# Performance work log

Measured on AMD Instinct MI355X. Metric: run time of the kernel, lower is better.

Reference implementation:

```python
import jax, jax.numpy as jnp
import numpy as np

# SMPL-style 22-joint kinematic tree; parents[i] < i for i >= 2 as the module's loop requires.
PARENTS = np.array([-1, 0, 0, 0, 1, 2, 3, 4, 5, 6, 7, 8, 9, 9, 9, 12, 13, 14, 16, 17, 18, 19])
L, J, D6 = 65536, 22, 6


def cont6d_to_mat(d6):
    """6D continuous rotation -> 3x3 rotation matrix (Gram-Schmidt). Columns are b1,b2,b3."""
    a1, a2 = d6[..., :3], d6[..., 3:]
    b1 = a1 / jnp.maximum(jnp.linalg.norm(a1, axis=-1, keepdims=True), 1e-12)
    b2 = a2 - b1 * jnp.sum(b1 * a2, axis=-1, keepdims=True)
    b2 = b2 / jnp.maximum(jnp.linalg.norm(b2, axis=-1, keepdims=True), 1e-12)
    b3 = jnp.cross(b1, b2)
    return jnp.stack((b1, b2, b3), axis=-1)  # (..., 3, 3)


def setup_inputs() -> dict:
    key = jax.random.key(0)
    k1, k2 = jax.random.split(key)
    pred_series = jax.random.normal(k1, (L, J, D6), dtype=jnp.float32)
    offsets = 0.1 * jax.random.normal(k2, (J, 3), dtype=jnp.float32)  # bone offsets (buffer)
    return {"pred_series": pred_series, "offsets": offsets}


def reference(pred_series, offsets):
    # pred_series: (L, 22, 6) -> global positions (L, 22, 3)
    rot_mats = cont6d_to_mat(pred_series)          # (L, 22, 3, 3)

    # Cumulative root rotation: R_t = R_{t-1} @ delta_t, R_{-1} = I  (sequential scan over time)
    deltas = rot_mats[:, 1]                        # (L, 3, 3)
    def step(R, d):
        Rn = R @ d
        return Rn, Rn
    _, R = jax.lax.scan(step, jnp.eye(3, dtype=pred_series.dtype), deltas)  # (L, 3, 3)

    # Root translation: integrate rotated local velocities
    vel_local = pred_series[:, 0, :3]              # (L, 3)
    global_vel = jnp.einsum('tij,tj->ti', R, vel_local)
    root_pos = jnp.cumsum(global_vel, axis=0)      # (L, 3)

    # FK down the static tree, vectorized over time; unrolled over 22 joints (static).
    rots = [None] * J
    pos = [None] * J
    rots[0], pos[0] = R, root_pos
    rots[1] = R
    pos[1] = pos[0] + jnp.einsum('tij,j->ti', R, offsets[1])
    for i in range(2, J):
        p = int(PARENTS[i])
        rots[i] = jnp.einsum('tij,tjk->tik', rots[p], rot_mats[:, i])
        pos[i] = pos[p] + jnp.einsum('tij,j->ti', rots[p], offsets[i])
    return jnp.stack(pos, axis=1)                  # (L, 22, 3)
```

## Files before the change

kernel.cpp:

```cpp
#include <hip/hip_runtime.h>
#include <hip/hip_bf16.h>
#include <stdint.h>


#define LTOT 65536
#define ROW 132
#define P1B 256
#define NBLK (LTOT / P1B)

struct Aff { float A[9]; float b[3]; };

__device__ __forceinline__ void d6_to_mat(float a0, float a1, float a2,
                                          float a3, float a4, float a5,
                                          float R[9]) {
  float n1 = sqrtf(a0 * a0 + a1 * a1 + a2 * a2);
  float i1 = 1.0f / fmaxf(n1, 1e-12f);
  float b10 = a0 * i1, b11 = a1 * i1, b12 = a2 * i1;
  float d = b10 * a3 + b11 * a4 + b12 * a5;
  float c0 = a3 - d * b10, c1 = a4 - d * b11, c2 = a5 - d * b12;
  float n2 = sqrtf(c0 * c0 + c1 * c1 + c2 * c2);
  float i2 = 1.0f / fmaxf(n2, 1e-12f);
  float b20 = c0 * i2, b21 = c1 * i2, b22 = c2 * i2;
  float b30 = b11 * b22 - b12 * b21;
  float b31 = b12 * b20 - b10 * b22;
  float b32 = b10 * b21 - b11 * b20;
  R[0] = b10; R[1] = b20; R[2] = b30;
  R[3] = b11; R[4] = b21; R[5] = b31;
  R[6] = b12; R[7] = b22; R[8] = b32;
}

__device__ __forceinline__ void mat_mul(const float A[9], const float B[9], float C[9]) {
#pragma unroll
  for (int i = 0; i < 3; ++i)
#pragma unroll
    for (int j = 0; j < 3; ++j)
      C[i * 3 + j] = A[i * 3 + 0] * B[0 + j] + A[i * 3 + 1] * B[3 + j] + A[i * 3 + 2] * B[6 + j];
}

__device__ __forceinline__ void mat_vec(const float A[9], float x, float y, float z,
                                        float& ox, float& oy, float& oz) {
  ox = A[0] * x + A[1] * y + A[2] * z;
  oy = A[3] * x + A[4] * y + A[5] * z;
  oz = A[6] * x + A[7] * y + A[8] * z;
}

__device__ __forceinline__ void compose(const Aff& P, const Aff& T, Aff& O) {
  mat_mul(P.A, T.A, O.A);
  float bx, by, bz;
  mat_vec(P.A, T.b[0], T.b[1], T.b[2], bx, by, bz);
  O.b[0] = P.b[0] + bx; O.b[1] = P.b[1] + by; O.b[2] = P.b[2] + bz;
}

__device__ __forceinline__ void aff_identity(Aff& v) {
  v.A[0] = 1.f; v.A[1] = 0.f; v.A[2] = 0.f;
  v.A[3] = 0.f; v.A[4] = 1.f; v.A[5] = 0.f;
  v.A[6] = 0.f; v.A[7] = 0.f; v.A[8] = 1.f;
  v.b[0] = 0.f; v.b[1] = 0.f; v.b[2] = 0.f;
}

__device__ __forceinline__ void wave_scan(Aff& v, int lane) {
#pragma unroll
  for (int s = 1; s < 64; s <<= 1) {
    Aff u;
#pragma unroll
    for (int k = 0; k < 9; ++k) u.A[k] = __shfl_up(v.A[k], s, 64);
#pragma unroll
    for (int k = 0; k < 3; ++k) u.b[k] = __shfl_up(v.b[k], s, 64);
    if (lane >= s) { Aff t; compose(u, v, t); v = t; }
  }
}

__global__ __launch_bounds__(P1B) void fk_phase1(const float* __restrict__ pred,
                                                 float* __restrict__ loc,
                                                 float* __restrict__ agg) {
  int t = blockIdx.x * P1B + threadIdx.x;
  int lane = threadIdx.x & 63, wid = threadIdx.x >> 6;

  const float4* q4 = (const float4*)(pred + (size_t)t * ROW);
  float4 qa = q4[0];
  float4 qb = q4[1];
  float4 qc = q4[2];
  Aff v;
  d6_to_mat(qb.z, qb.w, qc.x, qc.y, qc.z, qc.w, v.A);
  mat_vec(v.A, qa.x, qa.y, qa.z, v.b[0], v.b[1], v.b[2]);

  wave_scan(v, lane);

  __shared__ float sagg[P1B / 64][12];
  if (lane == 63) {
#pragma unroll
    for (int k = 0; k < 9; ++k) sagg[wid][k] = v.A[k];
#pragma unroll
    for (int k = 0; k < 3; ++k) sagg[wid][9 + k] = v.b[k];
  }
  __syncthreads();

  Aff pre; aff_identity(pre);
  for (int w = 0; w < wid; ++w) {
    Aff g, t2;
#pragma unroll
    for (int k = 0; k < 9; ++k) g.A[k] = sagg[w][k];
#pragma unroll
    for (int k = 0; k < 3; ++k) g.b[k] = sagg[w][9 + k];
    compose(pre, g, t2); pre = t2;
  }
  Aff f; compose(pre, v, f);

  float4* o = (float4*)(loc + (size_t)t * 12);
  o[0] = make_float4(f.A[0], f.A[1], f.A[2], f.A[3]);
  o[1] = make_float4(f.A[4], f.A[5], f.A[6], f.A[7]);
  o[2] = make_float4(f.A[8], f.b[0], f.b[1], f.b[2]);
  if (threadIdx.x == P1B - 1) {
    float4* a = (float4*)(agg + (size_t)blockIdx.x * 12);
    a[0] = make_float4(f.A[0], f.A[1], f.A[2], f.A[3]);
    a[1] = make_float4(f.A[4], f.A[5], f.A[6], f.A[7]);
    a[2] = make_float4(f.A[8], f.b[0], f.b[1], f.b[2]);
  }
}

__global__ __launch_bounds__(NBLK) void fk_phase2(const float* __restrict__ agg,
                                                  float* __restrict__ excl) {
  int i = threadIdx.x, lane = i & 63, wid = i >> 6;
  Aff v;
  {
    const float4* a = (const float4*)(agg + (size_t)i * 12);
    float4 a0 = a[0], a1 = a[1], a2 = a[2];
    v.A[0] = a0.x; v.A[1] = a0.y; v.A[2] = a0.z; v.A[3] = a0.w;
    v.A[4] = a1.x; v.A[5] = a1.y; v.A[6] = a1.z; v.A[7] = a1.w;
    v.A[8] = a2.x; v.b[0] = a2.y; v.b[1] = a2.z; v.b[2] = a2.w;
  }
  wave_scan(v, lane);

  __shared__ float sagg[NBLK / 64][12];
  if (lane == 63) {
#pragma unroll
    for (int k = 0; k < 9; ++k) sagg[wid][k] = v.A[k];
#pragma unroll
    for (int k = 0; k < 3; ++k) sagg[wid][9 + k] = v.b[k];
  }
  __syncthreads();

  Aff pre; aff_identity(pre);
  for (int w = 0; w < wid; ++w) {
    Aff g, t2;
#pragma unroll
    for (int k = 0; k < 9; ++k) g.A[k] = sagg[w][k];
#pragma unroll
    for (int k = 0; k < 3; ++k) g.b[k] = sagg[w][9 + k];
    compose(pre, g, t2); pre = t2;
  }
  Aff f; compose(pre, v, f);

  Aff e;
#pragma unroll
  for (int k = 0; k < 9; ++k) e.A[k] = __shfl_up(f.A[k], 1, 64);
#pragma unroll
  for (int k = 0; k < 3; ++k) e.b[k] = __shfl_up(f.b[k], 1, 64);
  if (lane == 0) e = pre;

  float4* o = (float4*)(excl + (size_t)i * 12);
  o[0] = make_float4(e.A[0], e.A[1], e.A[2], e.A[3]);
  o[1] = make_float4(e.A[4], e.A[5], e.A[6], e.A[7]);
  o[2] = make_float4(e.A[8], e.b[0], e.b[1], e.b[2]);
}

__global__ __launch_bounds__(256) void fk_phase3(const float* __restrict__ pred,
                                                 const float* __restrict__ offs,
                                                 const float* __restrict__ loc,
                                                 const float* __restrict__ excl,
                                                 float* __restrict__ out) {
  int t = blockIdx.x * blockDim.x + threadIdx.x;
  const float* lp = loc + (size_t)t * 12;
  const float* ep = excl + (size_t)(t / P1B) * 12;
  float Rl[9], Re[9];
#pragma unroll
  for (int k = 0; k < 9; ++k) { Rl[k] = lp[k]; Re[k] = ep[k]; }
  float R[9];
  mat_mul(Re, Rl, R);
  float rx, ry, rz;
  mat_vec(Re, lp[9], lp[10], lp[11], rx, ry, rz);
  float ov[66];
  ov[0] = ep[9] + rx; ov[1] = ep[10] + ry; ov[2] = ep[11] + rz;

  const float* q = pred + (size_t)t * ROW;

#define CHILD(j, p, Rp)                                                        \
  {                                                                            \
    float ox, oy, oz;                                                          \
    mat_vec(Rp, offs[(j)*3 + 0], offs[(j)*3 + 1], offs[(j)*3 + 2], ox, oy, oz);\
    ov[(j)*3 + 0] = ov[(p)*3 + 0] + ox;                                        \
    ov[(j)*3 + 1] = ov[(p)*3 + 1] + oy;                                        \
    ov[(j)*3 + 2] = ov[(p)*3 + 2] + oz;                                        \
  }
#define ROTJ(j, Rp, Rj)                                                        \
  {                                                                            \
    float Mx[9];                                                               \
    d6_to_mat(q[(j)*6 + 0], q[(j)*6 + 1], q[(j)*6 + 2], q[(j)*6 + 3],          \
              q[(j)*6 + 4], q[(j)*6 + 5], Mx);                                 \
    mat_mul(Rp, Mx, Rj);                                                       \
  }

  CHILD(1, 0, R);
  float r2[9], r3[9], r4[9];
  CHILD(2, 0, R); ROTJ(2, R, r2);
  CHILD(3, 0, R); ROTJ(3, R, r3);
  CHILD(4, 1, R); ROTJ(4, R, r4);
  float r5[9], r6[9], r7[9];
  CHILD(5, 2, r2); ROTJ(5, r2, r5);
  CHILD(6, 3, r3); ROTJ(6, r3, r6);
  CHILD(7, 4, r4); ROTJ(7, r4, r7);
  float r8[9], r9[9];
  CHILD(8, 5, r5); ROTJ(8, r5, r8);
  CHILD(9, 6, r6); ROTJ(9, r6, r9);
  CHILD(10, 7, r7);
  CHILD(11, 8, r8);
  float r12[9], r13[9], r14[9];
  CHILD(12, 9, r9); ROTJ(12, r9, r12);
  CHILD(13, 9, r9); ROTJ(13, r9, r13);
  CHILD(14, 9, r9); ROTJ(14, r9, r14);
  CHILD(15, 12, r12);
  float r16[9], r17[9];
  CHILD(16, 13, r13); ROTJ(16, r13, r16);
  CHILD(17, 14, r14); ROTJ(17, r14, r17);
  float r18[9], r19[9];
  CHILD(18, 16, r16); ROTJ(18, r16, r18);
  CHILD(19, 17, r17); ROTJ(19, r17, r19);
  CHILD(20, 18, r18);
  CHILD(21, 19, r19);

  float2* ob = (float2*)(out + (size_t)t * 66);
#pragma unroll
  for (int k = 0; k < 33; ++k) ob[k] = make_float2(ov[2 * k], ov[2 * k + 1]);
#undef CHILD
#undef ROTJ
}

extern "C" void kernel_launch(void* const* d_in, const int* in_sizes, int n_in,
                              void* d_out, int out_size, void* d_ws, size_t ws_size,
                              hipStream_t stream) {
  const float* pred = (const float*)d_in[0];
  const float* offs = (const float*)d_in[1];
  float* out = (float*)d_out;

  float* ws = (float*)d_ws;
  float* loc  = ws;
  float* agg  = ws + (size_t)12 * LTOT;
  float* excl = ws + (size_t)12 * LTOT + 12 * NBLK;

  fk_phase1<<<NBLK, P1B, 0, stream>>>(pred, loc, agg);
  fk_phase2<<<1, NBLK, 0, stream>>>(agg, excl);
  fk_phase3<<<LTOT / 256, 256, 0, stream>>>(pred, offs, loc, excl, out);
}
```

Measured before the change: 98.90 us.

## Fuse three scan/FK kernels into one cooperative kernel with grid sync

Replaces the three-launch scan pipeline with a single cooperative kernel. Each block computes its local scan, publishes its aggregate, waits at a grid-wide sync, and then redundantly scans all 256 block aggregates in shared memory to get its own prefix before running FK. This drops the per-thread loc buffer round trip and two kernel launches, and it loads the joint 6D values as float2. In exchange every block repeats the aggregate scan, the grid sync must be honoured, and the launch is restricted to one block per CU.

```diff
diff --git a/kernel.cpp b/kernel.cpp
--- a/kernel.cpp
+++ b/kernel.cpp
@@ -1,6 +1,8 @@
 #include <hip/hip_runtime.h>
-#include <hip/hip_bf16.h>
+#include <hip/hip_cooperative_groups.h>
 #include <stdint.h>
+
+namespace cg = cooperative_groups;
 
 
 #define LTOT 65536
@@ -70,11 +72,40 @@
   }
 }
 
-__global__ __launch_bounds__(P1B) void fk_phase1(const float* __restrict__ pred,
-                                                 float* __restrict__ loc,
-                                                 float* __restrict__ agg) {
-  int t = blockIdx.x * P1B + threadIdx.x;
-  int lane = threadIdx.x & 63, wid = threadIdx.x >> 6;
+__device__ __forceinline__ void block_scan(Aff& v, int lane, int wid,
+                                           float (*sagg)[12], Aff& f) {
+  wave_scan(v, lane);
+  if (lane == 63) {
+#pragma unroll
+    for (int k = 0; k < 9; ++k) sagg[wid][k] = v.A[k];
+#pragma unroll
+    for (int k = 0; k < 3; ++k) sagg[wid][9 + k] = v.b[k];
+  }
+  __syncthreads();
+  Aff pre; aff_identity(pre);
+  for (int w = 0; w < wid; ++w) {
+    Aff g, t2;
+#pragma unroll
+    for (int k = 0; k < 9; ++k) g.A[k] = sagg[w][k];
+#pragma unroll
+    for (int k = 0; k < 3; ++k) g.b[k] = sagg[w][9 + k];
+    compose(pre, g, t2); pre = t2;
+  }
+  compose(pre, v, f);
+}
+
+__global__ __launch_bounds__(P1B, 1) void fk_fused(const float* __restrict__ pred,
+                                                   const float* __restrict__ offs,
+                                                   float* __restrict__ agg,
+                                                   float* __restrict__ out) {
+  cg::grid_group grid = cg::this_grid();
+  int tid = threadIdx.x;
+  int t = blockIdx.x * P1B + tid;
+  int lane = tid & 63, wid = tid >> 6;
+
+  __shared__ float sagg1[P1B / 64][12];
+  __shared__ float sagg2[P1B / 64][12];
+  __shared__ float sincl[NBLK][13];
 
   const float4* q4 = (const float4*)(pred + (size_t)t * ROW);
   float4 qa = q4[0];
@@ -84,103 +115,50 @@
   d6_to_mat(qb.z, qb.w, qc.x, qc.y, qc.z, qc.w, v.A);
   mat_vec(v.A, qa.x, qa.y, qa.z, v.b[0], v.b[1], v.b[2]);
 
-  wave_scan(v, lane);
-
-  __shared__ float sagg[P1B / 64][12];
-  if (lane == 63) {
-#pragma unroll
-    for (int k = 0; k < 9; ++k) sagg[wid][k] = v.A[k];
-#pragma unroll
-    for (int k = 0; k < 3; ++k) sagg[wid][9 + k] = v.b[k];
-  }
-  __syncthreads();
-
-  Aff pre; aff_identity(pre);
-  for (int w = 0; w < wid; ++w) {
-    Aff g, t2;
-#pragma unroll
-    for (int k = 0; k < 9; ++k) g.A[k] = sagg[w][k];
-#pragma unroll
-    for (int k = 0; k < 3; ++k) g.b[k] = sagg[w][9 + k];
-    compose(pre, g, t2); pre = t2;
-  }
-  Aff f; compose(pre, v, f);
-
-  float4* o = (float4*)(loc + (size_t)t * 12);
-  o[0] = make_float4(f.A[0], f.A[1], f.A[2], f.A[3]);
-  o[1] = make_float4(f.A[4], f.A[5], f.A[6], f.A[7]);
-  o[2] = make_float4(f.A[8], f.b[0], f.b[1], f.b[2]);
-  if (threadIdx.x == P1B - 1) {
+  Aff f;
+  block_scan(v, lane, wid, sagg1, f);
+
+  if (tid == P1B - 1) {
     float4* a = (float4*)(agg + (size_t)blockIdx.x * 12);
     a[0] = make_float4(f.A[0], f.A[1], f.A[2], f.A[3]);
     a[1] = make_float4(f.A[4], f.A[5], f.A[6], f.A[7]);
     a[2] = make_float4(f.A[8], f.b[0], f.b[1], f.b[2]);
   }
-}
-
-__global__ __launch_bounds__(NBLK) void fk_phase2(const float* __restrict__ agg,
-                                                  float* __restrict__ excl) {
-  int i = threadIdx.x, lane = i & 63, wid = i >> 6;
-  Aff v;
+  __threadfence();
+  grid.sync();
+
+  Aff v2;
   {
-    const float4* a = (const float4*)(agg + (size_t)i * 12);
+    const float4* a = (const float4*)(agg + (size_t)tid * 12);
     float4 a0 = a[0], a1 = a[1], a2 = a[2];
-    v.A[0] = a0.x; v.A[1] = a0.y; v.A[2] = a0.z; v.A[3] = a0.w;
-    v.A[4] = a1.x; v.A[5] = a1.y; v.A[6] = a1.z; v.A[7] = a1.w;
-    v.A[8] = a2.x; v.b[0] = a2.y; v.b[1] = a2.z; v.b[2] = a2.w;
-  }
-  wave_scan(v, lane);
-
-  __shared__ float sagg[NBLK / 64][12];
-  if (lane == 63) {
-#pragma unroll
-    for (int k = 0; k < 9; ++k) sagg[wid][k] = v.A[k];
-#pragma unroll
-    for (int k = 0; k < 3; ++k) sagg[wid][9 + k] = v.b[k];
-  }
+    v2.A[0] = a0.x; v2.A[1] = a0.y; v2.A[2] = a0.z; v2.A[3] = a0.w;
+    v2.A[4] = a1.x; v2.A[5] = a1.y; v2.A[6] = a1.z; v2.A[7] = a1.w;
+    v2.A[8] = a2.x; v2.b[0] = a2.y; v2.b[1] = a2.z; v2.b[2] = a2.w;
+  }
+  Aff incl;
+  block_scan(v2, lane, wid, sagg2, incl);
+#pragma unroll
+  for (int k = 0; k < 9; ++k) sincl[tid][k] = incl.A[k];
+#pragma unroll
+  for (int k = 0; k < 3; ++k) sincl[tid][9 + k] = incl.b[k];
   __syncthreads();
 
-  Aff pre; aff_identity(pre);
-  for (int w = 0; w < wid; ++w) {
-    Aff g, t2;
-#pragma unroll
-    for (int k = 0; k < 9; ++k) g.A[k] = sagg[w][k];
-#pragma unroll
-    for (int k = 0; k < 3; ++k) g.b[k] = sagg[w][9 + k];
-    compose(pre, g, t2); pre = t2;
-  }
-  Aff f; compose(pre, v, f);
-
-  Aff e;
-#pragma unroll
-  for (int k = 0; k < 9; ++k) e.A[k] = __shfl_up(f.A[k], 1, 64);
-#pragma unroll
-  for (int k = 0; k < 3; ++k) e.b[k] = __shfl_up(f.b[k], 1, 64);
-  if (lane == 0) e = pre;
-
-  float4* o = (float4*)(excl + (size_t)i * 12);
-  o[0] = make_float4(e.A[0], e.A[1], e.A[2], e.A[3]);
-  o[1] = make_float4(e.A[4], e.A[5], e.A[6], e.A[7]);
-  o[2] = make_float4(e.A[8], e.b[0], e.b[1], e.b[2]);
-}
-
-__global__ __launch_bounds__(256) void fk_phase3(const float* __restrict__ pred,
-                                                 const float* __restrict__ offs,
-                                                 const float* __restrict__ loc,
-                                                 const float* __restrict__ excl,
-                                                 float* __restrict__ out) {
-  int t = blockIdx.x * blockDim.x + threadIdx.x;
-  const float* lp = loc + (size_t)t * 12;
-  const float* ep = excl + (size_t)(t / P1B) * 12;
-  float Rl[9], Re[9];
-#pragma unroll
-  for (int k = 0; k < 9; ++k) { Rl[k] = lp[k]; Re[k] = ep[k]; }
-  float R[9];
-  mat_mul(Re, Rl, R);
-  float rx, ry, rz;
-  mat_vec(Re, lp[9], lp[10], lp[11], rx, ry, rz);
+  Aff eb;
+  if (blockIdx.x == 0) {
+    aff_identity(eb);
+  } else {
+    const float* sp = sincl[blockIdx.x - 1];
+#pragma unroll
+    for (int k = 0; k < 9; ++k) eb.A[k] = sp[k];
+#pragma unroll
+    for (int k = 0; k < 3; ++k) eb.b[k] = sp[9 + k];
+  }
+
+  Aff g;
+  compose(eb, f, g);
+  const float* R = g.A;
   float ov[66];
-  ov[0] = ep[9] + rx; ov[1] = ep[10] + ry; ov[2] = ep[11] + rz;
+  ov[0] = g.b[0]; ov[1] = g.b[1]; ov[2] = g.b[2];
 
   const float* q = pred + (size_t)t * ROW;
 
@@ -194,9 +172,10 @@
   }
 #define ROTJ(j, Rp, Rj)                                                        \
   {                                                                            \
+    const float2* qq = (const float2*)(q + (j)*6);             \
+    float2 w0 = qq[0], w1 = qq[1], w2 = qq[2];                                 \
     float Mx[9];                                                               \
-    d6_to_mat(q[(j)*6 + 0], q[(j)*6 + 1], q[(j)*6 + 2], q[(j)*6 + 3],          \
-              q[(j)*6 + 4], q[(j)*6 + 5], Mx);                                 \
+    d6_to_mat(w0.x, w0.y, w1.x, w1.y, w2.x, w2.y, Mx);                         \
     mat_mul(Rp, Mx, Rj);                                                       \
   }
 
@@ -241,13 +220,9 @@
   const float* pred = (const float*)d_in[0];
   const float* offs = (const float*)d_in[1];
   float* out = (float*)d_out;
-
-  float* ws = (float*)d_ws;
-  float* loc  = ws;
-  float* agg  = ws + (size_t)12 * LTOT;
-  float* excl = ws + (size_t)12 * LTOT + 12 * NBLK;
-
-  fk_phase1<<<NBLK, P1B, 0, stream>>>(pred, loc, agg);
-  fk_phase2<<<1, NBLK, 0, stream>>>(agg, excl);
-  fk_phase3<<<LTOT / 256, 256, 0, stream>>>(pred, offs, loc, excl, out);
-}
+  float* agg = (float*)d_ws;
+
+  void* args[] = { (void*)&pred, (void*)&offs, (void*)&agg, (void*)&out };
+  hipLaunchCooperativeKernel((void*)fk_fused, dim3(NBLK), dim3(P1B),
+                             args, 0, stream);
+}
```

Measured after the change: 139.5 us. +41.1%, slower.

## Split tree FK pass into five per-chain waves per time step

Applied to the files above, without the earlier changes.

The final forward-kinematics kernel now launches 64x5 thread blocks. Each threadIdx.y row walks one kinematic chain of the skeleton for 64 time steps, instead of one thread evaluating all 22 joints serially. This targets the long dependent chain and high register pressure of the single-thread tree walk, giving more threads and more latency hiding. The cost is redundant work: every chain recomputes the root composition, and two chains recompute the spine joints 3, 6 and 9. Output stores are now scattered scalar writes. The scan kernels are refactored into a shared block_scan helper, and the second-level scan redundantly recomputes the prefix loop.

```diff
diff --git a/kernel.cpp b/kernel.cpp
--- a/kernel.cpp
+++ b/kernel.cpp
@@ -1,12 +1,11 @@
 #include <hip/hip_runtime.h>
-#include <hip/hip_bf16.h>
 #include <stdint.h>
 
 
 #define LTOT 65536
 #define ROW 132
 #define P1B 256
-#define NBLK (LTOT / P1B)
+#define NSCB (LTOT / P1B)
 
 struct Aff { float A[9]; float b[3]; };
 
@@ -70,11 +69,35 @@
   }
 }
 
-__global__ __launch_bounds__(P1B) void fk_phase1(const float* __restrict__ pred,
-                                                 float* __restrict__ loc,
-                                                 float* __restrict__ agg) {
-  int t = blockIdx.x * P1B + threadIdx.x;
-  int lane = threadIdx.x & 63, wid = threadIdx.x >> 6;
+__device__ __forceinline__ void block_scan(Aff& v, int lane, int wid,
+                                           float (*sagg)[12], Aff& f) {
+  wave_scan(v, lane);
+  if (lane == 63) {
+#pragma unroll
+    for (int k = 0; k < 9; ++k) sagg[wid][k] = v.A[k];
+#pragma unroll
+    for (int k = 0; k < 3; ++k) sagg[wid][9 + k] = v.b[k];
+  }
+  __syncthreads();
+  Aff pre; aff_identity(pre);
+  for (int w = 0; w < wid; ++w) {
+    Aff g, t2;
+#pragma unroll
+    for (int k = 0; k < 9; ++k) g.A[k] = sagg[w][k];
+#pragma unroll
+    for (int k = 0; k < 3; ++k) g.b[k] = sagg[w][9 + k];
+    compose(pre, g, t2); pre = t2;
+  }
+  compose(pre, v, f);
+}
+
+__global__ __launch_bounds__(P1B) void fk_scan(const float* __restrict__ pred,
+                                               float* __restrict__ loc,
+                                               float* __restrict__ agg) {
+  int tid = threadIdx.x;
+  int t = blockIdx.x * P1B + tid;
+  int lane = tid & 63, wid = tid >> 6;
+  __shared__ float sagg[P1B / 64][12];
 
   const float4* q4 = (const float4*)(pred + (size_t)t * ROW);
   float4 qa = q4[0];
@@ -83,34 +106,14 @@
   Aff v;
   d6_to_mat(qb.z, qb.w, qc.x, qc.y, qc.z, qc.w, v.A);
   mat_vec(v.A, qa.x, qa.y, qa.z, v.b[0], v.b[1], v.b[2]);
-
-  wave_scan(v, lane);
-
-  __shared__ float sagg[P1B / 64][12];
-  if (lane == 63) {
-#pragma unroll
-    for (int k = 0; k < 9; ++k) sagg[wid][k] = v.A[k];
-#pragma unroll
-    for (int k = 0; k < 3; ++k) sagg[wid][9 + k] = v.b[k];
-  }
-  __syncthreads();
-
-  Aff pre; aff_identity(pre);
-  for (int w = 0; w < wid; ++w) {
-    Aff g, t2;
-#pragma unroll
-    for (int k = 0; k < 9; ++k) g.A[k] = sagg[w][k];
-#pragma unroll
-    for (int k = 0; k < 3; ++k) g.b[k] = sagg[w][9 + k];
-    compose(pre, g, t2); pre = t2;
-  }
-  Aff f; compose(pre, v, f);
+  Aff f;
+  block_scan(v, lane, wid, sagg, f);
 
   float4* o = (float4*)(loc + (size_t)t * 12);
   o[0] = make_float4(f.A[0], f.A[1], f.A[2], f.A[3]);
   o[1] = make_float4(f.A[4], f.A[5], f.A[6], f.A[7]);
   o[2] = make_float4(f.A[8], f.b[0], f.b[1], f.b[2]);
-  if (threadIdx.x == P1B - 1) {
+  if (tid == P1B - 1) {
     float4* a = (float4*)(agg + (size_t)blockIdx.x * 12);
     a[0] = make_float4(f.A[0], f.A[1], f.A[2], f.A[3]);
     a[1] = make_float4(f.A[4], f.A[5], f.A[6], f.A[7]);
@@ -118,8 +121,8 @@
   }
 }
 
-__global__ __launch_bounds__(NBLK) void fk_phase2(const float* __restrict__ agg,
-                                                  float* __restrict__ excl) {
+__global__ __launch_bounds__(NSCB) void fk_scan2(const float* __restrict__ agg,
+                                                 float* __restrict__ excl) {
   int i = threadIdx.x, lane = i & 63, wid = i >> 6;
   Aff v;
   {
@@ -129,17 +132,9 @@
     v.A[4] = a1.x; v.A[5] = a1.y; v.A[6] = a1.z; v.A[7] = a1.w;
     v.A[8] = a2.x; v.b[0] = a2.y; v.b[1] = a2.z; v.b[2] = a2.w;
   }
-  wave_scan(v, lane);
-
-  __shared__ float sagg[NBLK / 64][12];
-  if (lane == 63) {
-#pragma unroll
-    for (int k = 0; k < 9; ++k) sagg[wid][k] = v.A[k];
-#pragma unroll
-    for (int k = 0; k < 3; ++k) sagg[wid][9 + k] = v.b[k];
-  }
-  __syncthreads();
-
+  __shared__ float sagg[NSCB / 64][12];
+  Aff f;
+  block_scan(v, lane, wid, sagg, f);
   Aff pre; aff_identity(pre);
   for (int w = 0; w < wid; ++w) {
     Aff g, t2;
@@ -149,90 +144,129 @@
     for (int k = 0; k < 3; ++k) g.b[k] = sagg[w][9 + k];
     compose(pre, g, t2); pre = t2;
   }
-  Aff f; compose(pre, v, f);
-
   Aff e;
 #pragma unroll
   for (int k = 0; k < 9; ++k) e.A[k] = __shfl_up(f.A[k], 1, 64);
 #pragma unroll
   for (int k = 0; k < 3; ++k) e.b[k] = __shfl_up(f.b[k], 1, 64);
   if (lane == 0) e = pre;
-
   float4* o = (float4*)(excl + (size_t)i * 12);
   o[0] = make_float4(e.A[0], e.A[1], e.A[2], e.A[3]);
   o[1] = make_float4(e.A[4], e.A[5], e.A[6], e.A[7]);
   o[2] = make_float4(e.A[8], e.b[0], e.b[1], e.b[2]);
 }
 
-__global__ __launch_bounds__(256) void fk_phase3(const float* __restrict__ pred,
-                                                 const float* __restrict__ offs,
-                                                 const float* __restrict__ loc,
-                                                 const float* __restrict__ excl,
-                                                 float* __restrict__ out) {
-  int t = blockIdx.x * blockDim.x + threadIdx.x;
-  const float* lp = loc + (size_t)t * 12;
-  const float* ep = excl + (size_t)(t / P1B) * 12;
-  float Rl[9], Re[9];
-#pragma unroll
-  for (int k = 0; k < 9; ++k) { Rl[k] = lp[k]; Re[k] = ep[k]; }
-  float R[9];
-  mat_mul(Re, Rl, R);
-  float rx, ry, rz;
-  mat_vec(Re, lp[9], lp[10], lp[11], rx, ry, rz);
-  float ov[66];
-  ov[0] = ep[9] + rx; ov[1] = ep[10] + ry; ov[2] = ep[11] + rz;
-
+struct Rowv { float2 a, b, c; };
+__device__ __forceinline__ Rowv loadrow(const float* q, int j) {
+  const float2* p = (const float2*)(q + j * 6);
+  Rowv r; r.a = p[0]; r.b = p[1]; r.c = p[2]; return r;
+}
+__device__ __forceinline__ void rowmat(const Rowv& r, float M[9]) {
+  d6_to_mat(r.a.x, r.a.y, r.b.x, r.b.y, r.c.x, r.c.y, M);
+}
+__device__ __forceinline__ void childp(const float* Rp, const float* offs, int j,
+                                       float px, float py, float pz,
+                                       float& ox, float& oy, float& oz,
+                                       float* ob) {
+  float dx, dy, dz;
+  mat_vec(Rp, offs[j * 3], offs[j * 3 + 1], offs[j * 3 + 2], dx, dy, dz);
+  ox = px + dx; oy = py + dy; oz = pz + dz;
+  ob[j * 3] = ox; ob[j * 3 + 1] = oy; ob[j * 3 + 2] = oz;
+}
+
+__global__ __launch_bounds__(320, 4) void fk_tree(const float* __restrict__ pred,
+                                                  const float* __restrict__ offs,
+                                                  const float* __restrict__ loc,
+                                                  const float* __restrict__ excl,
+                                                  float* __restrict__ out) {
+  int lane = threadIdx.x;
+  int chain = threadIdx.y;
+  int t = blockIdx.x * 64 + lane;
+  int sb = blockIdx.x >> 2;
+
+  Aff e, l;
+  {
+    const float4* a = (const float4*)(excl + (size_t)sb * 12);
+    float4 a0 = a[0], a1 = a[1], a2 = a[2];
+    e.A[0] = a0.x; e.A[1] = a0.y; e.A[2] = a0.z; e.A[3] = a0.w;
+    e.A[4] = a1.x; e.A[5] = a1.y; e.A[6] = a1.z; e.A[7] = a1.w;
+    e.A[8] = a2.x; e.b[0] = a2.y; e.b[1] = a2.z; e.b[2] = a2.w;
+  }
+  {
+    const float4* a = (const float4*)(loc + (size_t)t * 12);
+    float4 a0 = a[0], a1 = a[1], a2 = a[2];
+    l.A[0] = a0.x; l.A[1] = a0.y; l.A[2] = a0.z; l.A[3] = a0.w;
+    l.A[4] = a1.x; l.A[5] = a1.y; l.A[6] = a1.z; l.A[7] = a1.w;
+    l.A[8] = a2.x; l.b[0] = a2.y; l.b[1] = a2.z; l.b[2] = a2.w;
+  }
+  Aff g;
+  compose(e, l, g);
+  const float* R = g.A;
+  float px = g.b[0], py = g.b[1], pz = g.b[2];
   const float* q = pred + (size_t)t * ROW;
-
-#define CHILD(j, p, Rp)                                                        \
-  {                                                                            \
-    float ox, oy, oz;                                                          \
-    mat_vec(Rp, offs[(j)*3 + 0], offs[(j)*3 + 1], offs[(j)*3 + 2], ox, oy, oz);\
-    ov[(j)*3 + 0] = ov[(p)*3 + 0] + ox;                                        \
-    ov[(j)*3 + 1] = ov[(p)*3 + 1] + oy;                                        \
-    ov[(j)*3 + 2] = ov[(p)*3 + 2] + oz;                                        \
-  }
-#define ROTJ(j, Rp, Rj)                                                        \
-  {                                                                            \
-    float Mx[9];                                                               \
-    d6_to_mat(q[(j)*6 + 0], q[(j)*6 + 1], q[(j)*6 + 2], q[(j)*6 + 3],          \
-              q[(j)*6 + 4], q[(j)*6 + 5], Mx);                                 \
-    mat_mul(Rp, Mx, Rj);                                                       \
-  }
-
-  CHILD(1, 0, R);
-  float r2[9], r3[9], r4[9];
-  CHILD(2, 0, R); ROTJ(2, R, r2);
-  CHILD(3, 0, R); ROTJ(3, R, r3);
-  CHILD(4, 1, R); ROTJ(4, R, r4);
-  float r5[9], r6[9], r7[9];
-  CHILD(5, 2, r2); ROTJ(5, r2, r5);
-  CHILD(6, 3, r3); ROTJ(6, r3, r6);
-  CHILD(7, 4, r4); ROTJ(7, r4, r7);
-  float r8[9], r9[9];
-  CHILD(8, 5, r5); ROTJ(8, r5, r8);
-  CHILD(9, 6, r6); ROTJ(9, r6, r9);
-  CHILD(10, 7, r7);
-  CHILD(11, 8, r8);
-  float r12[9], r13[9], r14[9];
-  CHILD(12, 9, r9); ROTJ(12, r9, r12);
-  CHILD(13, 9, r9); ROTJ(13, r9, r13);
-  CHILD(14, 9, r9); ROTJ(14, r9, r14);
-  CHILD(15, 12, r12);
-  float r16[9], r17[9];
-  CHILD(16, 13, r13); ROTJ(16, r13, r16);
-  CHILD(17, 14, r14); ROTJ(17, r14, r17);
-  float r18[9], r19[9];
-  CHILD(18, 16, r16); ROTJ(18, r16, r18);
-  CHILD(19, 17, r17); ROTJ(19, r17, r19);
-  CHILD(20, 18, r18);
-  CHILD(21, 19, r19);
-
-  float2* ob = (float2*)(out + (size_t)t * 66);
-#pragma unroll
-  for (int k = 0; k < 33; ++k) ob[k] = make_float2(ov[2 * k], ov[2 * k + 1]);
-#undef CHILD
-#undef ROTJ
+  float* ob = out + (size_t)t * 66;
+
+  float M[9], ra[9], rb[9];
+  if (chain == 0) {
+    Rowv w4 = loadrow(q, 4), w7 = loadrow(q, 7);
+    ob[0] = px; ob[1] = py; ob[2] = pz;
+    float p1x, p1y, p1z, p4x, p4y, p4z, p7x, p7y, p7z, dx, dy, dz;
+    childp(R, offs, 1, px, py, pz, p1x, p1y, p1z, ob);
+    rowmat(w4, M); mat_mul(R, M, ra);
+    childp(R, offs, 4, p1x, p1y, p1z, p4x, p4y, p4z, ob);
+    childp(ra, offs, 7, p4x, p4y, p4z, p7x, p7y, p7z, ob);
+    rowmat(w7, M); mat_mul(ra, M, rb);
+    childp(rb, offs, 10, p7x, p7y, p7z, dx, dy, dz, ob);
+  } else if (chain == 1) {
+    Rowv w2 = loadrow(q, 2), w5 = loadrow(q, 5), w8 = loadrow(q, 8);
+    float p2x, p2y, p2z, p5x, p5y, p5z, p8x, p8y, p8z, dx, dy, dz;
+    childp(R, offs, 2, px, py, pz, p2x, p2y, p2z, ob);
+    rowmat(w2, M); mat_mul(R, M, ra);
+    childp(ra, offs, 5, p2x, p2y, p2z, p5x, p5y, p5z, ob);
+    rowmat(w5, M); mat_mul(ra, M, rb);
+    childp(rb, offs, 8, p5x, p5y, p5z, p8x, p8y, p8z, ob);
+    rowmat(w8, M); mat_mul(rb, M, ra);
+    childp(ra, offs, 11, p8x, p8y, p8z, dx, dy, dz, ob);
+  } else if (chain == 2) {
+    Rowv w3 = loadrow(q, 3), w6 = loadrow(q, 6), w9 = loadrow(q, 9),
+         w12 = loadrow(q, 12);
+    float p3x, p3y, p3z, p6x, p6y, p6z, p9x, p9y, p9z;
+    float p12x, p12y, p12z, dx, dy, dz;
+    childp(R, offs, 3, px, py, pz, p3x, p3y, p3z, ob);
+    rowmat(w3, M); mat_mul(R, M, ra);
+    childp(ra, offs, 6, p3x, p3y, p3z, p6x, p6y, p6z, ob);
+    rowmat(w6, M); mat_mul(ra, M, rb);
+    childp(rb, offs, 9, p6x, p6y, p6z, p9x, p9y, p9z, ob);
+    rowmat(w9, M); mat_mul(rb, M, ra);
+    childp(ra, offs, 12, p9x, p9y, p9z, p12x, p12y, p12z, ob);
+    rowmat(w12, M); mat_mul(ra, M, rb);
+    childp(rb, offs, 15, p12x, p12y, p12z, dx, dy, dz, ob);
+  } else {
+    int jA = (chain == 3) ? 13 : 14;
+    int jB = (chain == 3) ? 16 : 17;
+    int jC = (chain == 3) ? 18 : 19;
+    int jD = (chain == 3) ? 20 : 21;
+    Rowv w3 = loadrow(q, 3), w6 = loadrow(q, 6), w9 = loadrow(q, 9);
+    Rowv wA = loadrow(q, jA), wB = loadrow(q, jB), wC = loadrow(q, jC);
+    float p3x, p3y, p3z, p6x, p6y, p6z, p9x, p9y, p9z;
+    float pAx, pAy, pAz, pBx, pBy, pBz, pCx, pCy, pCz, dx, dy, dz;
+    mat_vec(R, offs[9], offs[10], offs[11], dx, dy, dz);
+    p3x = px + dx; p3y = py + dy; p3z = pz + dz;
+    rowmat(w3, M); mat_mul(R, M, ra);
+    mat_vec(ra, offs[18], offs[19], offs[20], dx, dy, dz);
+    p6x = p3x + dx; p6y = p3y + dy; p6z = p3z + dz;
+    rowmat(w6, M); mat_mul(ra, M, rb);
+    mat_vec(rb, offs[27], offs[28], offs[29], dx, dy, dz);
+    p9x = p6x + dx; p9y = p6y + dy; p9z = p6z + dz;
+    rowmat(w9, M); mat_mul(rb, M, ra);
+    childp(ra, offs, jA, p9x, p9y, p9z, pAx, pAy, pAz, ob);
+    rowmat(wA, M); mat_mul(ra, M, rb);
+    childp(rb, offs, jB, pAx, pAy, pAz, pBx, pBy, pBz, ob);
+    rowmat(wB, M); mat_mul(rb, M, ra);
+    childp(ra, offs, jC, pBx, pBy, pBz, pCx, pCy, pCz, ob);
+    rowmat(wC, M); mat_mul(ra, M, rb);
+    childp(rb, offs, jD, pCx, pCy, pCz, dx, dy, dz, ob);
+  }
 }
 
 extern "C" void kernel_launch(void* const* d_in, const int* in_sizes, int n_in,
@@ -245,9 +279,9 @@
   float* ws = (float*)d_ws;
   float* loc  = ws;
   float* agg  = ws + (size_t)12 * LTOT;
-  float* excl = ws + (size_t)12 * LTOT + 12 * NBLK;
-
-  fk_phase1<<<NBLK, P1B, 0, stream>>>(pred, loc, agg);
-  fk_phase2<<<1, NBLK, 0, stream>>>(agg, excl);
-  fk_phase3<<<LTOT / 256, 256, 0, stream>>>(pred, offs, loc, excl, out);
-}
+  float* excl = ws + (size_t)12 * LTOT + 12 * NSCB;
+
+  fk_scan<<<NSCB, P1B, 0, stream>>>(pred, loc, agg);
+  fk_scan2<<<1, NSCB, 0, stream>>>(agg, excl);
+  fk_tree<<<LTOT / 64, dim3(64, 5), 0, stream>>>(pred, offs, loc, excl, out);
+}
```

After: 105.5 us. +6.7%, slower.
